# Performance work log

Measured on AMD Instinct MI355X. Metric: run time of the kernel, lower is better.

Reference implementation:

```python
import jax, jax.numpy as jnp
import numpy as np

N_NODES = 50000
N_EDGES = 800000
F_IN = 128   # in_feats
H = 256      # h_feats
C = 32       # num_classes
E_IN = 2     # raw edge feature dim
EPS = 1e-12  # F.normalize eps


def _lin_params(key, fan_in, fan_out):
    kw, kb = jax.random.split(key)
    bound = 1.0 / np.sqrt(fan_in)
    W = jax.random.uniform(kw, (fan_in, fan_out), jnp.float32, -bound, bound)
    b = jax.random.uniform(kb, (fan_out,), jnp.float32, -bound, bound)
    return W, b


def setup_inputs() -> dict:
    key = jax.random.key(0)
    ks = jax.random.split(key, 12)
    inp = {
        "node_feat": jax.random.normal(ks[0], (N_NODES, F_IN), jnp.float32),
        "edge_feat": jax.random.normal(ks[1], (N_EDGES, E_IN), jnp.float32),
        "src": jax.random.randint(ks[2], (N_EDGES,), 0, N_NODES, jnp.int32),
        "dst": jax.random.randint(ks[3], (N_EDGES,), 0, N_NODES, jnp.int32),
    }
    # conv1: SAGEConv(F_IN, H, 2, F_IN)
    inp["We1"], inp["be1"] = _lin_params(ks[4], E_IN, F_IN)        # e_linear
    inp["Wr1a"], inp["br1a"] = _lin_params(ks[5], F_IN, F_IN)      # reduce_linear1
    inp["Wr1b"], inp["br1b"] = _lin_params(ks[6], F_IN, F_IN)      # reduce_linear2
    inp["Wl1"], inp["bl1"] = _lin_params(ks[7], 2 * F_IN, H)       # linear1
    # conv2: SAGEConv(H, C, F_IN, H)
    inp["We2"], inp["be2"] = _lin_params(ks[8], F_IN, H)
    inp["Wr2a"], inp["br2a"] = _lin_params(ks[9], H, H)
    inp["Wr2b"], inp["br2b"] = _lin_params(ks[10], H, H)
    inp["Wl2"], inp["bl2"] = _lin_params(ks[11], 2 * H, C)
    return inp


def _sage_conv(h, e, src, dst, We, be, Wra, bra, Wrb, brb, Wl, bl):
    # edge weight transform
    w = e @ We + be                                    # [E, e_out]
    hs = h[src]                                        # [E, F] gather
    hd = h[dst]
    # per-edge cosine similarity (scalar per edge)
    sn = hs / jnp.maximum(jnp.linalg.norm(hs, axis=1, keepdims=True), EPS)
    dn = hd / jnp.maximum(jnp.linalg.norm(hd, axis=1, keepdims=True), EPS)
    cos = jnp.sum(sn * dn, axis=1, keepdims=True)      # [E, 1]
    m = cos * w * hs                                   # message [E, F]
    # mailbox MLP applied per-edge, then mean-reduce per dst node
    r = jax.nn.relu(m @ Wra + bra)
    r = jax.nn.relu(r @ Wrb + brb)
    s = jax.ops.segment_sum(r, dst, num_segments=N_NODES)
    cnt = jax.ops.segment_sum(jnp.ones((dst.shape[0], 1), r.dtype), dst,
                              num_segments=N_NODES)
    h_N = s / jnp.maximum(cnt, 1.0)                    # zero-degree nodes -> 0
    h_out = jnp.concatenate([h, h_N], axis=1) @ Wl + bl
    return h_out, w


def reference(node_feat, edge_feat, src, dst,
              We1, be1, Wr1a, br1a, Wr1b, br1b, Wl1, bl1,
              We2, be2, Wr2a, br2a, Wr2b, br2b, Wl2, bl2):
    h, e_h = _sage_conv(node_feat, edge_feat, src, dst,
                        We1, be1, Wr1a, br1a, Wr1b, br1b, Wl1, bl1)
    h, e_h = jax.nn.relu(h), jax.nn.relu(e_h)
    h, _ = _sage_conv(h, e_h, src, dst,
                      We2, be2, Wr2a, br2a, Wr2b, br2b, Wl2, bl2)
    return h  # [N_NODES, C] logits
```

## Files before the change

### kernel.cpp

```cpp
#include <hip/hip_runtime.h>
#include <math.h>

#define NN 50000
#define NE 800000

typedef short bf8 __attribute__((ext_vector_type(8)));
typedef short bf4v __attribute__((ext_vector_type(4)));
typedef short bf2v __attribute__((ext_vector_type(2)));
typedef float f4 __attribute__((ext_vector_type(4)));

__device__ __forceinline__ short f2b(float f) {
  unsigned int u = __float_as_uint(f);
  unsigned int r = (u + 0x7FFFu + ((u >> 16) & 1u)) >> 16;
  return (short)(unsigned short)r;
}
__device__ __forceinline__ float b2f(short s) {
  return __uint_as_float(((unsigned int)(unsigned short)s) << 16);
}
__device__ __forceinline__ f4 b2f4(bf4v p) {
  f4 v;
  v[0] = b2f(p[0]); v[1] = b2f(p[1]); v[2] = b2f(p[2]); v[3] = b2f(p[3]);
  return v;
}

__global__ __launch_bounds__(256) void wt_k(const float* __restrict__ in,
                                            short* __restrict__ out,
                                            int K, int N) {
  int i = blockIdx.x * 256 + threadIdx.x;
  if (i >= K * N) return;
  int n = i / K, k = i - n * K;
  out[i] = f2b(in[(size_t)k * N + n]);
}

__global__ __launch_bounds__(256) void cvt_k(const float* __restrict__ in,
                                             short* __restrict__ out, int n4) {
  int i = blockIdx.x * 256 + threadIdx.x;
  if (i >= n4) return;
  f4 v = *(const f4*)&in[(size_t)i * 4];
  bf4v p;
  p[0] = f2b(v[0]); p[1] = f2b(v[1]); p[2] = f2b(v[2]); p[3] = f2b(v[3]);
  *(bf4v*)&out[(size_t)i * 4] = p;
}

__global__ __launch_bounds__(256) void norm1_k(const short* __restrict__ nfb,
                                               float* __restrict__ invn) {
  const int node = blockIdx.x * 4 + (threadIdx.x >> 6);
  if (node >= NN) return;
  const int lane = threadIdx.x & 63;
  bf2v hb = *(const bf2v*)&nfb[(size_t)node * 128 + lane * 2];
  float h0 = b2f(hb[0]), h1v = b2f(hb[1]);
  float ss = fmaf(h0, h0, h1v * h1v);
#pragma unroll
  for (int o = 32; o >= 1; o >>= 1) ss += __shfl_xor(ss, o);
  if (lane == 0) invn[node] = 1.f / fmaxf(sqrtf(ss), 1e-12f);
}

__global__ __launch_bounds__(256) void norm2_k(const short* __restrict__ h1b,
                                               float* __restrict__ invn) {
  const int node = blockIdx.x * 4 + (threadIdx.x >> 6);
  if (node >= NN) return;
  const int lane = threadIdx.x & 63;
  f4 h = b2f4(*(const bf4v*)&h1b[(size_t)node * 256 + lane * 4]);
  float ss = 0.f;
#pragma unroll
  for (int r = 0; r < 4; ++r) ss = fmaf(h[r], h[r], ss);
#pragma unroll
  for (int o = 32; o >= 1; o >>= 1) ss += __shfl_xor(ss, o);
  if (lane == 0) invn[node] = 1.f / fmaxf(sqrtf(ss), 1e-12f);
}

__global__ __launch_bounds__(256) void cnt_k(const int* __restrict__ dst,
                                             int* __restrict__ cnt) {
  int e = blockIdx.x * 256 + threadIdx.x;
  if (e >= NE) return;
  atomicAdd(&cnt[dst[e]], 1);
}

__global__ __launch_bounds__(1024) void scan_k(const int* __restrict__ cnt,
                                               int* __restrict__ off2) {
  __shared__ int buf[1024];
  __shared__ int carry_s;
  const int t = threadIdx.x;
  if (t == 0) carry_s = 0;
  __syncthreads();
  const int nch = (NN + 1023) / 1024;
  for (int ch = 0; ch < nch; ++ch) {
    const int i = ch * 1024 + t;
    const int v = (i < NN) ? cnt[i] : 0;
    buf[t] = v;
    __syncthreads();
#pragma unroll
    for (int o = 1; o < 1024; o <<= 1) {
      int x = (t >= o) ? buf[t - o] : 0;
      __syncthreads();
      buf[t] += x;
      __syncthreads();
    }
    const int incl = buf[t];
    const int carry = carry_s;
    if (i < NN) off2[i] = carry + incl - v;
    __syncthreads();
    if (t == 1023) carry_s = carry + incl;
    __syncthreads();
  }
}

__global__ __launch_bounds__(256) void perm_k(const int* __restrict__ dst,
                                              int* __restrict__ off2,
                                              int* __restrict__ perm,
                                              int* __restrict__ dsts) {
  int e = blockIdx.x * 256 + threadIdx.x;
  if (e >= NE) return;
  int d = dst[e];
  int p = atomicAdd(&off2[d], 1);
  perm[p] = e;
  dsts[p] = d;
}


__global__ __launch_bounds__(512, 8) void edge_mlp1(
    const short* __restrict__ nfb, const float* __restrict__ ef,
    const int* __restrict__ src, const int* __restrict__ perm,
    const int* __restrict__ dsts, const float* __restrict__ invn1,
    const float* __restrict__ We1, const float* __restrict__ be1,
    const short* __restrict__ WaT, const float* __restrict__ ba,
    const short* __restrict__ WbT, const float* __restrict__ bbv,
    float* __restrict__ s1)
{
  __shared__ __align__(16) short Ms[64 * 136];
  __shared__ int dse[64];
  __shared__ int sse[64];
  __shared__ float2 efs[64];
  const int t = threadIdx.x;
  const int e0 = blockIdx.x * 64;
  const int lane = t & 63, wv = t >> 6;

  if (t < 64) {
    const int pe = perm[e0 + t];
    dse[t] = dsts[e0 + t];
    sse[t] = src[pe];
    efs[t] = *(const float2*)&ef[2 * pe];
  }
  __syncthreads();

  {
    const int k2 = lane * 2;
    const float wA0 = We1[k2],       wA1 = We1[k2 + 1];
    const float wB0 = We1[128 + k2], wB1 = We1[128 + k2 + 1];
    const float bE0 = be1[k2],       bE1 = be1[k2 + 1];
    bf2v hbv[8], dbv[8];
#pragma unroll
    for (int i = 0; i < 8; ++i) {
      const int e = wv * 8 + i;
      hbv[i] = *(const bf2v*)&nfb[(size_t)sse[e] * 128 + k2];
      dbv[i] = *(const bf2v*)&nfb[(size_t)dse[e] * 128 + k2];
    }
#pragma unroll
    for (int i = 0; i < 8; ++i) {
      const int e = wv * 8 + i;
      const int s = sse[e];
      const int d = dse[e];
      const float h0 = b2f(hbv[i][0]), h1v = b2f(hbv[i][1]);
      const float g0 = b2f(dbv[i][0]), g1 = b2f(dbv[i][1]);
      float sd = fmaf(h0, g0, h1v * g1);
#pragma unroll
      for (int o = 32; o >= 1; o >>= 1) sd += __shfl_xor(sd, o);
      const float c = sd * invn1[s] * invn1[d];
      const float2 f01 = efs[e];
      const float w0 = fmaf(f01.x, wA0, fmaf(f01.y, wB0, bE0));
      const float w1 = fmaf(f01.x, wA1, fmaf(f01.y, wB1, bE1));
      bf2v pk;
      pk[0] = f2b(c * w0 * h0);
      pk[1] = f2b(c * w1 * h1v);
      *(bf2v*)&Ms[e * 136 + k2] = pk;
    }
  }
  __syncthreads();

  const int lr = lane & 15;
  const int lq = lane >> 4;
  const int n0 = wv * 16;

  f4 acc[4];
#pragma unroll
  for (int b = 0; b < 4; ++b) acc[b] = (f4)0.f;

#pragma unroll
  for (int kc = 0; kc < 128; kc += 32) {
    bf8 aF, bF[4];
    aF = *(const bf8*)&WaT[(size_t)(n0 + lr) * 128 + kc + lq * 8];
#pragma unroll
    for (int b = 0; b < 4; ++b)
      bF[b] = *(const bf8*)&Ms[(b * 16 + lr) * 136 + kc + lq * 8];
#pragma unroll
    for (int b = 0; b < 4; ++b)
      acc[b] = __builtin_amdgcn_mfma_f32_16x16x32_bf16(aF, bF[b], acc[b], 0, 0, 0);
  }
  __syncthreads();

  {
    const int n = n0 + lq * 4;
    f4 bb = *(const f4*)&ba[n];
#pragma unroll
    for (int b = 0; b < 4; ++b) {
      bf4v pk;
#pragma unroll
      for (int r = 0; r < 4; ++r) pk[r] = f2b(fmaxf(acc[b][r] + bb[r], 0.f));
      *(bf4v*)&Ms[(b * 16 + lr) * 136 + n] = pk;
    }
  }
  __syncthreads();

#pragma unroll
  for (int b = 0; b < 4; ++b) acc[b] = (f4)0.f;
#pragma unroll
  for (int kc = 0; kc < 128; kc += 32) {
    bf8 aF, bF[4];
    aF = *(const bf8*)&WbT[(size_t)(n0 + lr) * 128 + kc + lq * 8];
#pragma unroll
    for (int b = 0; b < 4; ++b)
      bF[b] = *(const bf8*)&Ms[(b * 16 + lr) * 136 + kc + lq * 8];
#pragma unroll
    for (int b = 0; b < 4; ++b)
      acc[b] = __builtin_amdgcn_mfma_f32_16x16x32_bf16(aF, bF[b], acc[b], 0, 0, 0);
  }
  __syncthreads();

  {
    const int n = n0 + lq * 4;
    f4 bb = *(const f4*)&bbv[n];
#pragma unroll
    for (int b = 0; b < 4; ++b) {
      bf4v pk;
#pragma unroll
      for (int r = 0; r < 4; ++r) pk[r] = f2b(fmaxf(acc[b][r] + bb[r], 0.f));
      *(bf4v*)&Ms[(b * 16 + lr) * 136 + n] = pk;
    }
  }
  __syncthreads();

  {
    const int f = t & 127;
    const int eb = (t >> 7) * 16;
    float vals[16];
#pragma unroll
    for (int j = 0; j < 16; ++j) vals[j] = b2f(Ms[(eb + j) * 136 + f]);
    float run = 0.f;
    int pd = dse[eb];
#pragma unroll
    for (int j = 0; j < 16; ++j) {
      const int d = dse[eb + j];
      if (d != pd) {
        atomicAdd(&s1[(size_t)pd * 128 + f], run);
        run = 0.f;
        pd = d;
      }
      run += vals[j];
    }
    atomicAdd(&s1[(size_t)pd * 128 + f], run);
  }
}


__global__ __launch_bounds__(512, 6) void edge_mlp2(
    const short* __restrict__ h1b, const float* __restrict__ ef,
    const int* __restrict__ src, const int* __restrict__ perm,
    const int* __restrict__ dsts, const float* __restrict__ invn2,
    const float* __restrict__ We1, const float* __restrict__ be1,
    const short* __restrict__ We2T, const float* __restrict__ be2,
    const short* __restrict__ WaT, const float* __restrict__ ba,
    const short* __restrict__ WbT, const float* __restrict__ bbv,
    float* __restrict__ s2)
{
  __shared__ __align__(16) short U[64 * 264];
  __shared__ int dse[64];
  __shared__ int pes[64];
  __shared__ int sse[64];
  short* Ws  = U;
  short* M2s = U;
  const int t = threadIdx.x;
  const int e0 = blockIdx.x * 64;
  const int lane = t & 63, wv = t >> 6;
  const int lr = lane & 15;
  const int lq = lane >> 4;
  const int n0 = wv * 32;

  if (t < 64) {
    const int pe = perm[e0 + t];
    pes[t] = pe;
    dse[t] = dsts[e0 + t];
    sse[t] = src[pe];
  }
  __syncthreads();

  {
    const int e = t >> 3;
    const int kb = (t & 7) * 16;
    const int pe = pes[e];
    const float f0 = ef[2 * pe], f1 = ef[2 * pe + 1];
#pragma unroll
    for (int j = 0; j < 2; ++j) {
      const int k = kb + j * 8;
      f4 wa0 = *(const f4*)&We1[k];
      f4 wa1 = *(const f4*)&We1[k + 4];
      f4 wb0 = *(const f4*)&We1[128 + k];
      f4 wb1 = *(const f4*)&We1[128 + k + 4];
      f4 b0 = *(const f4*)&be1[k];
      f4 b1 = *(const f4*)&be1[k + 4];
      bf8 pk;
#pragma unroll
      for (int x = 0; x < 4; ++x) {
        pk[x]     = f2b(fmaxf(fmaf(f0, wa0[x], fmaf(f1, wb0[x], b0[x])), 0.f));
        pk[x + 4] = f2b(fmaxf(fmaf(f0, wa1[x], fmaf(f1, wb1[x], b1[x])), 0.f));
      }
      *(bf8*)&Ws[e * 136 + k] = pk;
    }
  }
  __syncthreads();

  f4 acc[2][4];
#pragma unroll
  for (int a = 0; a < 2; ++a)
#pragma unroll
    for (int b = 0; b < 4; ++b) acc[a][b] = (f4)0.f;

#pragma unroll
  for (int kc = 0; kc < 128; kc += 32) {
    bf8 aF[2], bF[4];
#pragma unroll
    for (int a = 0; a < 2; ++a)
      aF[a] = *(const bf8*)&We2T[(size_t)(n0 + a * 16 + lr) * 128 + kc + lq * 8];
#pragma unroll
    for (int b = 0; b < 4; ++b)
      bF[b] = *(const bf8*)&Ws[(b * 16 + lr) * 136 + kc + lq * 8];
#pragma unroll
    for (int a = 0; a < 2; ++a)
#pragma unroll
      for (int b = 0; b < 4; ++b)
        acc[a][b] = __builtin_amdgcn_mfma_f32_16x16x32_bf16(aF[a], bF[b], acc[a][b], 0, 0, 0);
  }
  __syncthreads();

#pragma unroll
  for (int b = 0; b < 4; ++b) {
#pragma unroll
    for (int a = 0; a < 2; ++a) {
      const int n = n0 + a * 16 + lq * 4;
      f4 bb = *(const f4*)&be2[n];
      bf4v pk;
#pragma unroll
      for (int r = 0; r < 4; ++r) pk[r] = f2b(acc[a][b][r] + bb[r]);
      *(bf4v*)&M2s[(b * 16 + lr) * 264 + n] = pk;
    }
  }
  __syncthreads();

  {
    const int k4 = lane * 4;
    bf4v hsv[8], hdv[8];
#pragma unroll
    for (int i = 0; i < 8; ++i) {
      const int e = wv * 8 + i;
      hsv[i] = *(const bf4v*)&h1b[(size_t)sse[e] * 256 + k4];
      hdv[i] = *(const bf4v*)&h1b[(size_t)dse[e] * 256 + k4];
    }
#pragma unroll
    for (int i = 0; i < 8; ++i) {
      const int e = wv * 8 + i;
      const int s = sse[e];
      const int d = dse[e];
      f4 hs = b2f4(hsv[i]);
      f4 hd = b2f4(hdv[i]);
      float sd = 0.f;
#pragma unroll
      for (int r = 0; r < 4; ++r) sd = fmaf(hs[r], hd[r], sd);
#pragma unroll
      for (int o = 32; o >= 1; o >>= 1) sd += __shfl_xor(sd, o);
      const float c = sd * invn2[s] * invn2[d];
      f4 w = b2f4(*(const bf4v*)&M2s[e * 264 + k4]);
      bf4v pk;
#pragma unroll
      for (int r = 0; r < 4; ++r) pk[r] = f2b(w[r] * c * hs[r]);
      *(bf4v*)&M2s[e * 264 + k4] = pk;
    }
  }
  __syncthreads();

#pragma unroll
  for (int a = 0; a < 2; ++a)
#pragma unroll
    for (int b = 0; b < 4; ++b) acc[a][b] = (f4)0.f;
  for (int kc = 0; kc < 256; kc += 32) {
    bf8 aF[2], bF[4];
#pragma unroll
    for (int a = 0; a < 2; ++a)
      aF[a] = *(const bf8*)&WaT[(size_t)(n0 + a * 16 + lr) * 256 + kc + lq * 8];
#pragma unroll
    for (int b = 0; b < 4; ++b)
      bF[b] = *(const bf8*)&M2s[(b * 16 + lr) * 264 + kc + lq * 8];
#pragma unroll
    for (int a = 0; a < 2; ++a)
#pragma unroll
      for (int b = 0; b < 4; ++b)
        acc[a][b] = __builtin_amdgcn_mfma_f32_16x16x32_bf16(aF[a], bF[b], acc[a][b], 0, 0, 0);
  }
  __syncthreads();

#pragma unroll
  for (int a = 0; a < 2; ++a) {
    const int n = n0 + a * 16 + lq * 4;
    f4 bb = *(const f4*)&ba[n];
#pragma unroll
    for (int b = 0; b < 4; ++b) {
      bf4v pk;
#pragma unroll
      for (int r = 0; r < 4; ++r) pk[r] = f2b(fmaxf(acc[a][b][r] + bb[r], 0.f));
      *(bf4v*)&M2s[(b * 16 + lr) * 264 + n] = pk;
    }
  }
  __syncthreads();

#pragma unroll
  for (int a = 0; a < 2; ++a)
#pragma unroll
    for (int b = 0; b < 4; ++b) acc[a][b] = (f4)0.f;
  for (int kc = 0; kc < 256; kc += 32) {
    bf8 aF[2], bF[4];
#pragma unroll
    for (int a = 0; a < 2; ++a)
      aF[a] = *(const bf8*)&WbT[(size_t)(n0 + a * 16 + lr) * 256 + kc + lq * 8];
#pragma unroll
    for (int b = 0; b < 4; ++b)
      bF[b] = *(const bf8*)&M2s[(b * 16 + lr) * 264 + kc + lq * 8];
#pragma unroll
    for (int a = 0; a < 2; ++a)
#pragma unroll
      for (int b = 0; b < 4; ++b)
        acc[a][b] = __builtin_amdgcn_mfma_f32_16x16x32_bf16(aF[a], bF[b], acc[a][b], 0, 0, 0);
  }
  __syncthreads();

  float* RF = (float*)M2s;
#pragma unroll
  for (int h = 0; h < 2; ++h) {
    if ((wv >> 2) == h) {
#pragma unroll
      for (int a = 0; a < 2; ++a) {
        const int n = n0 + a * 16 + lq * 4;
        f4 bb = *(const f4*)&bbv[n];
#pragma unroll
        for (int b = 0; b < 4; ++b) {
          f4 v;
#pragma unroll
          for (int r = 0; r < 4; ++r) v[r] = fmaxf(acc[a][b][r] + bb[r], 0.f);
          *(f4*)&RF[(b * 16 + lr) * 132 + (n - h * 128)] = v;
        }
      }
    }
    __syncthreads();
    {
      const int f = t & 127;
      const int eb = (t >> 7) * 16;
      float run = 0.f;
      int pd = dse[eb];
#pragma unroll 4
      for (int e = eb; e < eb + 16; ++e) {
        const int d = dse[e];
        if (d != pd) {
          atomicAdd(&s2[(size_t)pd * 256 + h * 128 + f], run);
          run = 0.f;
          pd = d;
        }
        run += RF[e * 132 + f];
      }
      atomicAdd(&s2[(size_t)pd * 256 + h * 128 + f], run);
    }
    __syncthreads();
  }
}


__global__ __launch_bounds__(256, 3) void h1m_k(
    const float* __restrict__ nf, const float* __restrict__ s1,
    const int* __restrict__ cnt, const short* __restrict__ Wl1T,
    const float* __restrict__ bl1, short* __restrict__ h1b)
{
  __shared__ __align__(16) short As[64 * 264];
  const int t = threadIdx.x;
  const int v0 = blockIdx.x * 64;

  {
    const int row = t >> 2;
    const int kb = (t & 3) * 64;
    int gn = v0 + row;
    if (gn >= NN) gn = NN - 1;
    const float inv = 1.f / fmaxf((float)cnt[gn], 1.f);
#pragma unroll
    for (int j = 0; j < 64; j += 8) {
      const int k = kb + j;
      f4 x0, x1;
      if (k < 128) {
        x0 = *(const f4*)&nf[(size_t)gn * 128 + k];
        x1 = *(const f4*)&nf[(size_t)gn * 128 + k + 4];
      } else {
        x0 = *(const f4*)&s1[(size_t)gn * 128 + (k - 128)];
        x1 = *(const f4*)&s1[(size_t)gn * 128 + (k - 124)];
#pragma unroll
        for (int x = 0; x < 4; ++x) { x0[x] *= inv; x1[x] *= inv; }
      }
      bf8 pk;
#pragma unroll
      for (int x = 0; x < 4; ++x) { pk[x] = f2b(x0[x]); pk[x + 4] = f2b(x1[x]); }
      *(bf8*)&As[row * 264 + k] = pk;
    }
  }
  __syncthreads();

  const int lane = t & 63, wv = t >> 6;
  const int lr = lane & 15;
  const int lq = lane >> 4;
  const int n0 = wv * 64;

  f4 acc[4][4];
#pragma unroll
  for (int a = 0; a < 4; ++a)
#pragma unroll
    for (int b = 0; b < 4; ++b) acc[a][b] = (f4)0.f;

  for (int kc = 0; kc < 256; kc += 32) {
    bf8 aF[4], bF[4];
#pragma unroll
    for (int a = 0; a < 4; ++a)
      aF[a] = *(const bf8*)&Wl1T[(size_t)(n0 + a * 16 + lr) * 256 + kc + lq * 8];
#pragma unroll
    for (int b = 0; b < 4; ++b)
      bF[b] = *(const bf8*)&As[(b * 16 + lr) * 264 + kc + lq * 8];
#pragma unroll
    for (int a = 0; a < 4; ++a)
#pragma unroll
      for (int b = 0; b < 4; ++b)
        acc[a][b] = __builtin_amdgcn_mfma_f32_16x16x32_bf16(aF[a], bF[b], acc[a][b], 0, 0, 0);
  }

#pragma unroll
  for (int b = 0; b < 4; ++b) {
    const int gn = v0 + b * 16 + lr;
    if (gn >= NN) continue;
#pragma unroll
    for (int a = 0; a < 4; ++a) {
      const int n = n0 + a * 16 + lq * 4;
      f4 bb = *(const f4*)&bl1[n];
      bf4v pk;
      pk[0] = f2b(fmaxf(acc[a][b][0] + bb[0], 0.f));
      pk[1] = f2b(fmaxf(acc[a][b][1] + bb[1], 0.f));
      pk[2] = f2b(fmaxf(acc[a][b][2] + bb[2], 0.f));
      pk[3] = f2b(fmaxf(acc[a][b][3] + bb[3], 0.f));
      *(bf4v*)&h1b[(size_t)gn * 256 + n] = pk;
    }
  }
}


__global__ __launch_bounds__(256) void out_k(
    const short* __restrict__ h1b, const float* __restrict__ s2,
    const int* __restrict__ cnt, const float* __restrict__ Wl2,
    const float* __restrict__ bl2, float* __restrict__ out)
{
  __shared__ float A8[8][512];
  const int n0 = blockIdx.x * 8;
  const int tx = threadIdx.x;
  const int ty = threadIdx.y;
  const int t = ty * 32 + tx;
  const int row = t >> 5;
  const int k0 = (t & 31) * 16;
  const int n = n0 + row;
  const float inv = 1.0f / fmaxf((float)cnt[n], 1.0f);
#pragma unroll
  for (int i = 0; i < 16; i += 4) {
    int k = k0 + i;
    f4 v;
    if (k < 256) {
      v = b2f4(*(const bf4v*)&h1b[(size_t)n * 256 + k]);
    } else {
      v = *(const f4*)&s2[(size_t)n * 256 + (k - 256)];
      v[0] *= inv; v[1] *= inv; v[2] *= inv; v[3] *= inv;
    }
    *(f4*)&A8[row][k] = v;
  }
  __syncthreads();
  float acc = bl2[tx];
#pragma unroll 8
  for (int k = 0; k < 512; k++) acc = fmaf(A8[ty][k], Wl2[(size_t)k * 32 + tx], acc);
  out[(size_t)(n0 + ty) * 32 + tx] = acc;
}


extern "C" void kernel_launch(void* const* d_in, const int* in_sizes, int n_in,
                              void* d_out, int out_size, void* d_ws, size_t ws_size,
                              hipStream_t stream) {
  const float* nf   = (const float*)d_in[0];
  const float* ef   = (const float*)d_in[1];
  const int*   src  = (const int*)d_in[2];
  const int*   dst  = (const int*)d_in[3];
  const float* We1  = (const float*)d_in[4];
  const float* be1  = (const float*)d_in[5];
  const float* Wr1a = (const float*)d_in[6];
  const float* br1a = (const float*)d_in[7];
  const float* Wr1b = (const float*)d_in[8];
  const float* br1b = (const float*)d_in[9];
  const float* Wl1  = (const float*)d_in[10];
  const float* bl1  = (const float*)d_in[11];
  const float* We2  = (const float*)d_in[12];
  const float* be2  = (const float*)d_in[13];
  const float* Wr2a = (const float*)d_in[14];
  const float* br2a = (const float*)d_in[15];
  const float* Wr2b = (const float*)d_in[16];
  const float* br2b = (const float*)d_in[17];
  const float* Wl2  = (const float*)d_in[18];
  const float* bl2  = (const float*)d_in[19];

  float* ws = (float*)d_ws;
  float* s1   = ws;
  float* s2   = s1 + (size_t)NN * 128;
  int*   cnt  = (int*)(s2 + (size_t)NN * 256);
  short* h1b  = (short*)(cnt + NN);
  short* nfb  = h1b + (size_t)NN * 256;
  short* WaT1 = nfb + (size_t)NN * 128;
  short* WbT1 = WaT1 + 128 * 128;
  short* We2T = WbT1 + 128 * 128;
  short* WaT2 = We2T + 256 * 128;
  short* WbT2 = WaT2 + 256 * 256;
  short* Wl1T = WbT2 + 256 * 256;
  int*   off2 = (int*)(Wl1T + 256 * 256);
  int*   perm = off2 + NN;
  int*   dsts = perm + NE;
  float* invn1 = (float*)(dsts + NE);
  float* invn2 = invn1 + NN;

  size_t need = ((size_t)NN * 128 + (size_t)NN * 256 + NN) * 4 +
                ((size_t)NN * 256 + (size_t)NN * 128 +
                 (size_t)128 * 128 * 2 + (size_t)256 * 128 +
                 (size_t)256 * 256 * 3) * 2 +
                ((size_t)NN + 2 * (size_t)NE + 2 * (size_t)NN) * 4;
  if (ws_size < need) return;

  wt_k<<<(128 * 128 + 255) / 256, 256, 0, stream>>>(Wr1a, WaT1, 128, 128);
  wt_k<<<(128 * 128 + 255) / 256, 256, 0, stream>>>(Wr1b, WbT1, 128, 128);
  wt_k<<<(128 * 256 + 255) / 256, 256, 0, stream>>>(We2, We2T, 128, 256);
  wt_k<<<(256 * 256 + 255) / 256, 256, 0, stream>>>(Wr2a, WaT2, 256, 256);
  wt_k<<<(256 * 256 + 255) / 256, 256, 0, stream>>>(Wr2b, WbT2, 256, 256);
  wt_k<<<(256 * 256 + 255) / 256, 256, 0, stream>>>(Wl1, Wl1T, 256, 256);
  cvt_k<<<(NN * 128 / 4 + 255) / 256, 256, 0, stream>>>(nf, nfb, NN * 128 / 4);
  norm1_k<<<(NN + 3) / 4, 256, 0, stream>>>(nfb, invn1);

  hipMemsetAsync(s1, 0, ((size_t)NN * 128 + (size_t)NN * 256 + NN) * 4, stream);

  cnt_k<<<NE / 256, 256, 0, stream>>>(dst, cnt);

  scan_k<<<1, 1024, 0, stream>>>(cnt, off2);
  perm_k<<<NE / 256, 256, 0, stream>>>(dst, off2, perm, dsts);

  edge_mlp1<<<NE / 64, 512, 0, stream>>>(nfb, ef, src, perm, dsts, invn1,
                                         We1, be1, WaT1, br1a, WbT1, br1b, s1);

  h1m_k<<<(NN + 63) / 64, 256, 0, stream>>>(nf, s1, cnt, Wl1T, bl1, h1b);
  norm2_k<<<(NN + 3) / 4, 256, 0, stream>>>(h1b, invn2);

  edge_mlp2<<<NE / 64, 512, 0, stream>>>(h1b, ef, src, perm, dsts, invn2,
                                         We1, be1, We2T, be2, WaT2, br2a,
                                         WbT2, br2b, s2);

  out_k<<<NN / 8, dim3(32, 8), 0, stream>>>(h1b, s2, cnt, Wl2, bl2, (float*)d_out);
}
```

Before: 1.288 ms.

## Fuse prep kernels into one launch and parallelize degree prefix scan

```diff
diff --git a/kernel.cpp b/kernel.cpp
--- a/kernel.cpp
+++ b/kernel.cpp
@@ -23,23 +23,41 @@
   return v;
 }
 
-__global__ __launch_bounds__(256) void wt_k(const float* __restrict__ in,
-                                            short* __restrict__ out,
-                                            int K, int N) {
-  int i = blockIdx.x * 256 + threadIdx.x;
-  if (i >= K * N) return;
-  int n = i / K, k = i - n * K;
-  out[i] = f2b(in[(size_t)k * N + n]);
-}
-
-__global__ __launch_bounds__(256) void cvt_k(const float* __restrict__ in,
-                                             short* __restrict__ out, int n4) {
-  int i = blockIdx.x * 256 + threadIdx.x;
-  if (i >= n4) return;
-  f4 v = *(const f4*)&in[(size_t)i * 4];
-  bf4v p;
-  p[0] = f2b(v[0]); p[1] = f2b(v[1]); p[2] = f2b(v[2]); p[3] = f2b(v[3]);
-  *(bf4v*)&out[(size_t)i * 4] = p;
+
+__global__ __launch_bounds__(256) void prep_k(
+    const float* __restrict__ Wr1a, const float* __restrict__ Wr1b,
+    const float* __restrict__ We2,  const float* __restrict__ Wr2a,
+    const float* __restrict__ Wr2b, const float* __restrict__ Wl1,
+    short* __restrict__ WaT1, short* __restrict__ WbT1,
+    short* __restrict__ We2T, short* __restrict__ WaT2,
+    short* __restrict__ WbT2, short* __restrict__ Wl1T,
+    const float* __restrict__ nf, short* __restrict__ nfb,
+    const int* __restrict__ dst, int* __restrict__ cnt)
+{
+  const int b = blockIdx.x;
+  if (b < 1024) {
+    const float* in; short* out; int K, N, bb;
+    if (b < 64)       { in = Wr1a; out = WaT1; K = 128; N = 128; bb = b; }
+    else if (b < 128) { in = Wr1b; out = WbT1; K = 128; N = 128; bb = b - 64; }
+    else if (b < 256) { in = We2;  out = We2T; K = 128; N = 256; bb = b - 128; }
+    else if (b < 512) { in = Wr2a; out = WaT2; K = 256; N = 256; bb = b - 256; }
+    else if (b < 768) { in = Wr2b; out = WbT2; K = 256; N = 256; bb = b - 512; }
+    else              { in = Wl1;  out = Wl1T; K = 256; N = 256; bb = b - 768; }
+    const int i = bb * 256 + threadIdx.x;
+    if (i < K * N) {
+      const int n = i / K, k = i - n * K;
+      out[i] = f2b(in[(size_t)k * N + n]);
+    }
+  } else if (b < 7274) {
+    const int i = (b - 1024) * 256 + threadIdx.x;
+    f4 v = *(const f4*)&nf[(size_t)i * 4];
+    bf4v p;
+    p[0] = f2b(v[0]); p[1] = f2b(v[1]); p[2] = f2b(v[2]); p[3] = f2b(v[3]);
+    *(bf4v*)&nfb[(size_t)i * 4] = p;
+  } else {
+    const int e = (b - 7274) * 256 + threadIdx.x;
+    atomicAdd(&cnt[dst[e]], 1);
+  }
 }
 
 __global__ __launch_bounds__(256) void norm1_k(const short* __restrict__ nfb,
@@ -69,40 +87,44 @@
   if (lane == 0) invn[node] = 1.f / fmaxf(sqrtf(ss), 1e-12f);
 }
 
-__global__ __launch_bounds__(256) void cnt_k(const int* __restrict__ dst,
-                                             int* __restrict__ cnt) {
-  int e = blockIdx.x * 256 + threadIdx.x;
-  if (e >= NE) return;
-  atomicAdd(&cnt[dst[e]], 1);
-}
-
-__global__ __launch_bounds__(1024) void scan_k(const int* __restrict__ cnt,
-                                               int* __restrict__ off2) {
+
+__global__ __launch_bounds__(1024) void scanA_k(const int* __restrict__ cnt,
+                                                int* __restrict__ off2,
+                                                int* __restrict__ bsum) {
   __shared__ int buf[1024];
-  __shared__ int carry_s;
   const int t = threadIdx.x;
-  if (t == 0) carry_s = 0;
-  __syncthreads();
-  const int nch = (NN + 1023) / 1024;
-  for (int ch = 0; ch < nch; ++ch) {
-    const int i = ch * 1024 + t;
-    const int v = (i < NN) ? cnt[i] : 0;
-    buf[t] = v;
+  const int i = blockIdx.x * 1024 + t;
+  const int v = (i < NN) ? cnt[i] : 0;
+  buf[t] = v;
+  __syncthreads();
+#pragma unroll
+  for (int o = 1; o < 1024; o <<= 1) {
+    int x = (t >= o) ? buf[t - o] : 0;
     __syncthreads();
-#pragma unroll
-    for (int o = 1; o < 1024; o <<= 1) {
-      int x = (t >= o) ? buf[t - o] : 0;
-      __syncthreads();
-      buf[t] += x;
-      __syncthreads();
-    }
-    const int incl = buf[t];
-    const int carry = carry_s;
-    if (i < NN) off2[i] = carry + incl - v;
+    buf[t] += x;
     __syncthreads();
-    if (t == 1023) carry_s = carry + incl;
-    __syncthreads();
-  }
+  }
+  if (i < NN) off2[i] = buf[t] - v;
+  if (t == 1023) bsum[blockIdx.x] = buf[t];
+}
+
+__global__ __launch_bounds__(64) void scanB_k(int* __restrict__ bsum, int nb) {
+  const int t = threadIdx.x;
+  int v = (t < nb) ? bsum[t] : 0;
+#pragma unroll
+  for (int o = 1; o < 64; o <<= 1) {
+    int x = __shfl_up(v, o);
+    if (t >= o) v += x;
+  }
+  if (t < nb) bsum[t] = v;
+}
+
+__global__ __launch_bounds__(256) void scanC_k(int* __restrict__ off2,
+                                               const int* __restrict__ bsum) {
+  const int i = blockIdx.x * 256 + threadIdx.x;
+  if (i >= NN) return;
+  const int b = i >> 10;
+  if (b) off2[i] += bsum[b - 1];
 }
 
 __global__ __launch_bounds__(256) void perm_k(const int* __restrict__ dst,
@@ -636,28 +658,26 @@
   int*   dsts = perm + NE;
   float* invn1 = (float*)(dsts + NE);
   float* invn2 = invn1 + NN;
+  int*   bsum  = (int*)(invn2 + NN);
 
   size_t need = ((size_t)NN * 128 + (size_t)NN * 256 + NN) * 4 +
                 ((size_t)NN * 256 + (size_t)NN * 128 +
                  (size_t)128 * 128 * 2 + (size_t)256 * 128 +
                  (size_t)256 * 256 * 3) * 2 +
-                ((size_t)NN + 2 * (size_t)NE + 2 * (size_t)NN) * 4;
+                ((size_t)NN + 2 * (size_t)NE + 2 * (size_t)NN) * 4 + 64 * 4;
   if (ws_size < need) return;
 
-  wt_k<<<(128 * 128 + 255) / 256, 256, 0, stream>>>(Wr1a, WaT1, 128, 128);
-  wt_k<<<(128 * 128 + 255) / 256, 256, 0, stream>>>(Wr1b, WbT1, 128, 128);
-  wt_k<<<(128 * 256 + 255) / 256, 256, 0, stream>>>(We2, We2T, 128, 256);
-  wt_k<<<(256 * 256 + 255) / 256, 256, 0, stream>>>(Wr2a, WaT2, 256, 256);
-  wt_k<<<(256 * 256 + 255) / 256, 256, 0, stream>>>(Wr2b, WbT2, 256, 256);
-  wt_k<<<(256 * 256 + 255) / 256, 256, 0, stream>>>(Wl1, Wl1T, 256, 256);
-  cvt_k<<<(NN * 128 / 4 + 255) / 256, 256, 0, stream>>>(nf, nfb, NN * 128 / 4);
+  hipMemsetAsync(s1, 0, ((size_t)NN * 128 + (size_t)NN * 256 + NN) * 4, stream);
+
+  prep_k<<<10399, 256, 0, stream>>>(Wr1a, Wr1b, We2, Wr2a, Wr2b, Wl1,
+                                    WaT1, WbT1, We2T, WaT2, WbT2, Wl1T,
+                                    nf, nfb, dst, cnt);
   norm1_k<<<(NN + 3) / 4, 256, 0, stream>>>(nfb, invn1);
 
-  hipMemsetAsync(s1, 0, ((size_t)NN * 128 + (size_t)NN * 256 + NN) * 4, stream);
-
-  cnt_k<<<NE / 256, 256, 0, stream>>>(dst, cnt);
-
-  scan_k<<<1, 1024, 0, stream>>>(cnt, off2);
+  const int nb = (NN + 1023) / 1024;
+  scanA_k<<<nb, 1024, 0, stream>>>(cnt, off2, bsum);
+  scanB_k<<<1, 64, 0, stream>>>(bsum, nb);
+  scanC_k<<<(NN + 255) / 256, 256, 0, stream>>>(off2, bsum);
   perm_k<<<NE / 256, 256, 0, stream>>>(dst, off2, perm, dsts);
 
   edge_mlp1<<<NE / 64, 512, 0, stream>>>(nfb, ef, src, perm, dsts, invn1,
```

New measurement: 1.184 ms. 8.1% less time.
